# Optimization experiments

Measured on AMD Instinct MI355X. Metric: run time of the kernel, lower is better.

## Reference

```python
import jax, jax.numpy as jnp
import numpy as np

N = 100000      # nodes
E = 1600000     # edges (avg degree 16)
F_IN = 300      # input feature dim
H = 64          # hidden channels
OUT = 20        # output classes
L = 8           # num GCN2Conv layers
ALPHA = 0.1
THETA = 0.5


def setup_inputs() -> dict:
    key = jax.random.key(0)
    ks = jax.random.split(key, 6)
    x = jax.random.normal(ks[0], (N, F_IN), jnp.float32)
    edge_index = jax.random.randint(ks[1], (2, E), 0, N, dtype=jnp.int32)
    edge_weights = jax.random.uniform(ks[2], (E,), jnp.float32)
    W_in = jax.random.normal(ks[3], (F_IN, H), jnp.float32) / np.sqrt(F_IN)
    b_in = jnp.zeros((H,), jnp.float32)
    conv_w = jax.random.normal(ks[4], (L, H, H), jnp.float32) / np.sqrt(H)
    W_out = jax.random.normal(ks[5], (H, OUT), jnp.float32) / np.sqrt(H)
    b_out = jnp.zeros((OUT,), jnp.float32)
    return dict(x=x, edge_index=edge_index, edge_weights=edge_weights,
                W_in=W_in, b_in=b_in, conv_w=conv_w, W_out=W_out, b_out=b_out)


def _gcn_norm(edge_index, edge_weights, n, dtype):
    # add self-loops with weight 1, symmetric normalization (PyG gcn_norm)
    loop = jnp.arange(n, dtype=edge_index.dtype)
    row = jnp.concatenate([edge_index[0], loop])
    col = jnp.concatenate([edge_index[1], loop])
    w = jnp.concatenate([edge_weights, jnp.ones((n,), dtype)])
    deg = jax.ops.segment_sum(w, col, num_segments=n)
    dinv = jnp.where(deg > 0, jax.lax.rsqrt(deg), 0.0).astype(dtype)
    norm = dinv[row] * w * dinv[col]
    return row, col, norm


def reference(x, edge_index, edge_weights, W_in, b_in, conv_w, W_out, b_out):
    n = x.shape[0]
    row, col, norm = _gcn_norm(edge_index, edge_weights, n, x.dtype)
    # eval mode: dropout is identity
    h = jax.nn.relu(x @ W_in + b_in)   # start_with_lin (F_IN != H)
    x0 = h
    num_layers = conv_w.shape[0]
    for l in range(num_layers):
        beta = float(np.log(THETA / (l + 1) + 1.0))
        # A_hat @ h : gather sources, weight by norm, scatter-add to targets
        agg = jax.ops.segment_sum(norm[:, None] * h[row], col, num_segments=n)
        z = (1.0 - ALPHA) * agg + ALPHA * x0  # initial-residual mixing
        h = jax.nn.relu((1.0 - beta) * z + beta * (z @ conv_w[l]))
    return h @ W_out + b_out
```

## Files before the change

### kernel.cpp

```cpp
#include <hip/hip_runtime.h>
#include <hip/hip_fp16.h>
#include <math.h>


#define HID 64
#define FIN 300
#define NOUT 20
#define ALPHA 0.1f
#define DSCALE 262144.0f
#define CNT_SHIFT 25
#define DEG_MASK 0x1FFFFFFu

typedef _Float16 f16;
typedef f16 f16x8 __attribute__((ext_vector_type(8)));
typedef float f32x4 __attribute__((ext_vector_type(4)));

__device__ __forceinline__ float wdec(unsigned v) {
    union { unsigned short u; __half h; } c;
    c.u = (unsigned short)(v >> 17);
    return __half2float(c.h);
}

__global__ void accum_k(const int* __restrict__ row, const int* __restrict__ col,
                        const float* __restrict__ ew,
                        unsigned* __restrict__ packed,
                        uint2* __restrict__ rec, int e) {
    int i = blockIdx.x * blockDim.x + threadIdx.x;
    if (i < e) {
        int c = col[i], r = row[i];
        float wv = ew[i];
        unsigned q = (unsigned)__float2uint_rn(wv * DSCALE);
        unsigned old = atomicAdd(&packed[c], (1u << CNT_SHIFT) | q);
        unsigned rank = (old >> CNT_SHIFT) & 0x7Fu;
        union { __half h; unsigned short u; } cv;
        cv.h = __float2half(wv);
        rec[i] = make_uint2((unsigned)c | (rank << 17),
                            (unsigned)r | ((unsigned)cv.u << 17));
    }
}

__global__ __launch_bounds__(1024) void unpackscan_k(const unsigned* __restrict__ packed,
                                                     float* __restrict__ dinv,
                                                     int* __restrict__ padcnt,
                                                     int* __restrict__ bsum, int n) {
    __shared__ int ws[16];
    int t = threadIdx.x, i = blockIdx.x * 1024 + t;
    int pad = 0;
    if (i < n) {
        unsigned v = packed[i];
        int cnt = (int)(v >> CNT_SHIFT);
        float d = 1.0f + (float)(v & DEG_MASK) * (1.0f / DSCALE);
        dinv[i] = rsqrtf(d);
        pad = (cnt + 3) & ~3;
        padcnt[i] = pad;
    }
    int s = pad;
#pragma unroll
    for (int d = 1; d < 64; d <<= 1) s += __shfl_xor(s, d);
    if ((t & 63) == 0) ws[t >> 6] = s;
    __syncthreads();
    if (t == 0) {
        int tot = 0;
#pragma unroll
        for (int k = 0; k < 16; ++k) tot += ws[k];
        bsum[blockIdx.x] = tot;
    }
}

__global__ void scan2_k(int* __restrict__ bsum, int nb, int* __restrict__ rp, int n) {
    int lane = threadIdx.x;
    int acc = 0;
    for (int base = 0; base < nb; base += 64) {
        int idx = base + lane;
        int orig = (idx < nb) ? bsum[idx] : 0;
        int v = orig;
#pragma unroll
        for (int d = 1; d < 64; d <<= 1) {
            int u = __shfl_up(v, d);
            if (lane >= d) v += u;
        }
        if (idx < nb) bsum[idx] = acc + v - orig;
        acc += __shfl(v, 63);
    }
    if (lane == 0) rp[n] = acc;
}

__global__ __launch_bounds__(1024) void scan3_k(const int* __restrict__ padcnt,
                                                const int* __restrict__ bsum,
                                                int* __restrict__ rp, int n) {
    __shared__ int ws[16];
    int t = threadIdx.x, i = blockIdx.x * 1024 + t;
    int lane = t & 63, w = t >> 6;
    int v = (i < n) ? padcnt[i] : 0;
    int sv = v;
#pragma unroll
    for (int d = 1; d < 64; d <<= 1) {
        int u = __shfl_up(sv, d);
        if (lane >= d) sv += u;
    }
    if (lane == 63) ws[w] = sv;
    __syncthreads();
    if (w == 0) {
        int x = (lane < 16) ? ws[lane] : 0;
#pragma unroll
        for (int d = 1; d < 16; d <<= 1) {
            int u = __shfl_up(x, d);
            if (lane >= d) x += u;
        }
        if (lane < 16) ws[lane] = x;
    }
    __syncthreads();
    int woff = (w > 0) ? ws[w - 1] : 0;
    if (i < n) rp[i] = bsum[blockIdx.x] + woff + sv - v;
}

__global__ __launch_bounds__(256) void fill_k(const uint2* __restrict__ rec,
                                              const float* __restrict__ dinv,
                                              const int* __restrict__ rp,
                                              unsigned* __restrict__ edges,
                                              int e, int n) {
    int xcd = blockIdx.x & 7;
    int lo = (int)(((long long)n * xcd) >> 3);
    int hi = (int)(((long long)n * (xcd + 1)) >> 3);
    int nblk = gridDim.x >> 3;
    int stride = nblk * 256;
    for (int i = (blockIdx.x >> 3) * 256 + threadIdx.x; i < e; i += stride) {
        uint2 rc = rec[i];
        int c = (int)(rc.x & 0x1FFFFu);
        if (c < lo || c >= hi) continue;
        int r = (int)(rc.y & 0x1FFFFu);
        union { unsigned short u; __half h; } ev;
        ev.u = (unsigned short)(rc.y >> 17);
        float nw = (1.0f - ALPHA) * dinv[r] * __half2float(ev.h) * dinv[c];
        union { __half h; unsigned short u; } cv;
        cv.h = __float2half(nw);
        int rank = (int)((rc.x >> 17) & 0x7Fu);
        int pos = rp[c] + rank;
        edges[pos] = ((unsigned)cv.u << 17) | (unsigned)r;
    }
}

__global__ void wt_k(const float* __restrict__ Win, f16* __restrict__ Wt) {
    int i = blockIdx.x * blockDim.x + threadIdx.x;
    if (i < 64 * 320) {
        int c = i / 320, k = i - c * 320;
        Wt[i] = (k < FIN) ? (f16)Win[k * 64 + c] : (f16)0.0f;
    }
}

__global__ __launch_bounds__(256) void gemm_in_k(const float* __restrict__ x,
                                                 const f16* __restrict__ Wt,
                                                 const float* __restrict__ bin,
                                                 __half* __restrict__ x0h, int n) {
    __shared__ f16 As[64 * 72];
    int t = threadIdx.x, lane = t & 63, wv = t >> 6;
    int node0 = blockIdx.x * 64;
    int lr = lane & 15, kg = lane >> 4;
    int fi = t & 15, rowbase = t >> 4;
    f32x4 acc0 = {0, 0, 0, 0}, acc1 = {0, 0, 0, 0}, acc2 = {0, 0, 0, 0}, acc3 = {0, 0, 0, 0};
    float4 xr[4];

    auto loadchunk = [&](int c) {
#pragma unroll
        for (int it = 0; it < 4; ++it) {
            int row = rowbase + it * 16;
            int rr = node0 + row;
            rr = (rr < n) ? rr : (n - 1);
            int kbase = c * 64 + fi * 4;
            xr[it] = make_float4(0.f, 0.f, 0.f, 0.f);
            if (kbase < FIN)
                xr[it] = *reinterpret_cast<const float4*>(x + (size_t)rr * FIN + kbase);
        }
    };
    loadchunk(0);

    for (int c = 0; c < 5; ++c) {
        __syncthreads();
#pragma unroll
        for (int it = 0; it < 4; ++it) {
            int row = rowbase + it * 16;
            union { float2 f2; f16 h[4]; } u;
            u.h[0] = (f16)xr[it].x; u.h[1] = (f16)xr[it].y;
            u.h[2] = (f16)xr[it].z; u.h[3] = (f16)xr[it].w;
            *reinterpret_cast<float2*>(As + row * 72 + fi * 4) = u.f2;
        }
        __syncthreads();
        if (c < 4) loadchunk(c + 1);
#pragma unroll
        for (int ks = 0; ks < 2; ++ks) {
            f16x8 a = *(const f16x8*)(As + (wv * 16 + lr) * 72 + ks * 32 + kg * 8);
            const f16* wb = Wt + c * 64 + ks * 32 + kg * 8;
            f16x8 b0 = *(const f16x8*)(wb + (0 * 16 + lr) * 320);
            f16x8 b1 = *(const f16x8*)(wb + (1 * 16 + lr) * 320);
            f16x8 b2 = *(const f16x8*)(wb + (2 * 16 + lr) * 320);
            f16x8 b3 = *(const f16x8*)(wb + (3 * 16 + lr) * 320);
            acc0 = __builtin_amdgcn_mfma_f32_16x16x32_f16(a, b0, acc0, 0, 0, 0);
            acc1 = __builtin_amdgcn_mfma_f32_16x16x32_f16(a, b1, acc1, 0, 0, 0);
            acc2 = __builtin_amdgcn_mfma_f32_16x16x32_f16(a, b2, acc2, 0, 0, 0);
            acc3 = __builtin_amdgcn_mfma_f32_16x16x32_f16(a, b3, acc3, 0, 0, 0);
        }
    }
    float bi0 = bin[0 * 16 + lr], bi1 = bin[1 * 16 + lr];
    float bi2 = bin[2 * 16 + lr], bi3 = bin[3 * 16 + lr];
    f16 ov[4][4];
#pragma unroll
    for (int r = 0; r < 4; ++r) {
        ov[0][r] = (f16)fmaxf(acc0[r] + bi0, 0.f);
        ov[1][r] = (f16)fmaxf(acc1[r] + bi1, 0.f);
        ov[2][r] = (f16)fmaxf(acc2[r] + bi2, 0.f);
        ov[3][r] = (f16)fmaxf(acc3[r] + bi3, 0.f);
    }
    __syncthreads();
#pragma unroll
    for (int cg = 0; cg < 4; ++cg)
#pragma unroll
        for (int r = 0; r < 4; ++r)
            As[(wv * 16 + kg * 4 + r) * 72 + cg * 16 + lr] = ov[cg][r];
    __syncthreads();
#pragma unroll
    for (int it = 0; it < 2; ++it) {
        int idx = t + it * 256;
        int ch = idx & 3, nodel = (idx >> 2) & 63, q = idx >> 8;
        int node = node0 + nodel;
        if (node < n)
            *(float4*)((f16*)x0h + ((size_t)q * n + node) * 32 + ch * 8) =
                *reinterpret_cast<const float4*>(As + nodel * 72 + q * 32 + ch * 8);
    }
}

__global__ __launch_bounds__(256) void layer_k(const int* __restrict__ rp,
                                               const unsigned* __restrict__ edges,
                                               const float* __restrict__ dinv,
                                               const __half* __restrict__ x0h,
                                               const __half* __restrict__ hin,
                                               __half* __restrict__ hout,
                                               const float* __restrict__ Wl,
                                               float beta, int n,
                                               const float* __restrict__ Wout,
                                               const float* __restrict__ bout,
                                               float* __restrict__ out) {
    __shared__ f16 As[64 * 72];
    __shared__ f16 Bs[64 * 72];
    int t = threadIdx.x, lane = t & 63, wv = t >> 6;
    int node0 = blockIdx.x * 64;
    for (int i = t; i < 4096; i += 256) {
        int k = i >> 6, c = i & 63;
        Bs[c * 72 + k] = (f16)Wl[i];
    }
    int g = lane >> 2, s = lane & 3;
    int row = wv * 16 + g;
    int node = node0 + row;
    int nd = (node < n) ? node : (n - 1);
    int jbeg = rp[nd], end = (node < n) ? rp[nd + 1] : jbeg;
    float di = dinv[nd];
    float c1 = (1.0f - ALPHA) * di * di;
#pragma unroll
    for (int q = 0; q < 2; ++q) {
        const f16* hp = (const f16*)hin + (size_t)q * n * 32;
        const f16* xp = (const f16*)x0h + (size_t)q * n * 32;
        float a0[8], a1[8], a2[8], a3[8];
#pragma unroll
        for (int i = 0; i < 8; ++i) { a0[i] = 0.f; a1[i] = 0.f; a2[i] = 0.f; a3[i] = 0.f; }
        int j = jbeg;
        while (__any(j < end)) {
            if (j < end) {
                uint4 e4 = *reinterpret_cast<const uint4*>(edges + j);
                float w0 = wdec(e4.x), w1 = wdec(e4.y), w2 = wdec(e4.z), w3 = wdec(e4.w);
                f16x8 r0 = *(const f16x8*)(hp + (size_t)(e4.x & 0x1FFFF) * 32 + s * 8);
                f16x8 r1 = *(const f16x8*)(hp + (size_t)(e4.y & 0x1FFFF) * 32 + s * 8);
                f16x8 r2 = *(const f16x8*)(hp + (size_t)(e4.z & 0x1FFFF) * 32 + s * 8);
                f16x8 r3 = *(const f16x8*)(hp + (size_t)(e4.w & 0x1FFFF) * 32 + s * 8);
#pragma unroll
                for (int i = 0; i < 8; ++i) {
                    a0[i] = fmaf(w0, (float)r0[i], a0[i]);
                    a1[i] = fmaf(w1, (float)r1[i], a1[i]);
                    a2[i] = fmaf(w2, (float)r2[i], a2[i]);
                    a3[i] = fmaf(w3, (float)r3[i], a3[i]);
                }
            }
            j += 4;
        }
        f16x8 h8 = *(const f16x8*)(hp + (size_t)nd * 32 + s * 8);
        f16x8 x8 = *(const f16x8*)(xp + (size_t)nd * 32 + s * 8);
        f16x8 z8;
#pragma unroll
        for (int i = 0; i < 8; ++i)
            z8[i] = (f16)fmaf(ALPHA, (float)x8[i],
                              fmaf(c1, (float)h8[i], (a0[i] + a1[i]) + (a2[i] + a3[i])));
        *(f16x8*)(As + row * 72 + q * 32 + s * 8) = z8;
    }
    __syncthreads();
    int lr = lane & 15, kg = lane >> 4;
    f32x4 acc0 = {0, 0, 0, 0}, acc1 = {0, 0, 0, 0}, acc2 = {0, 0, 0, 0}, acc3 = {0, 0, 0, 0};
    f16x8 af0 = *(const f16x8*)(As + (wv * 16 + lr) * 72 + kg * 8);
    f16x8 af1 = *(const f16x8*)(As + (wv * 16 + lr) * 72 + 32 + kg * 8);
    {
        f16x8 b0 = *(const f16x8*)(Bs + (0 * 16 + lr) * 72 + kg * 8);
        f16x8 b1 = *(const f16x8*)(Bs + (0 * 16 + lr) * 72 + 32 + kg * 8);
        acc0 = __builtin_amdgcn_mfma_f32_16x16x32_f16(af0, b0, acc0, 0, 0, 0);
        acc0 = __builtin_amdgcn_mfma_f32_16x16x32_f16(af1, b1, acc0, 0, 0, 0);
    }
    {
        f16x8 b0 = *(const f16x8*)(Bs + (1 * 16 + lr) * 72 + kg * 8);
        f16x8 b1 = *(const f16x8*)(Bs + (1 * 16 + lr) * 72 + 32 + kg * 8);
        acc1 = __builtin_amdgcn_mfma_f32_16x16x32_f16(af0, b0, acc1, 0, 0, 0);
        acc1 = __builtin_amdgcn_mfma_f32_16x16x32_f16(af1, b1, acc1, 0, 0, 0);
    }
    {
        f16x8 b0 = *(const f16x8*)(Bs + (2 * 16 + lr) * 72 + kg * 8);
        f16x8 b1 = *(const f16x8*)(Bs + (2 * 16 + lr) * 72 + 32 + kg * 8);
        acc2 = __builtin_amdgcn_mfma_f32_16x16x32_f16(af0, b0, acc2, 0, 0, 0);
        acc2 = __builtin_amdgcn_mfma_f32_16x16x32_f16(af1, b1, acc2, 0, 0, 0);
    }
    {
        f16x8 b0 = *(const f16x8*)(Bs + (3 * 16 + lr) * 72 + kg * 8);
        f16x8 b1 = *(const f16x8*)(Bs + (3 * 16 + lr) * 72 + 32 + kg * 8);
        acc3 = __builtin_amdgcn_mfma_f32_16x16x32_f16(af0, b0, acc3, 0, 0, 0);
        acc3 = __builtin_amdgcn_mfma_f32_16x16x32_f16(af1, b1, acc3, 0, 0, 0);
    }
    float omb = 1.0f - beta;
    f16 ov[4][4];
#pragma unroll
    for (int cg = 0; cg < 4; ++cg) {
        f32x4 acc = (cg == 0) ? acc0 : (cg == 1) ? acc1 : (cg == 2) ? acc2 : acc3;
        int col = cg * 16 + lr;
#pragma unroll
        for (int r = 0; r < 4; ++r) {
            float zv = (float)As[(wv * 16 + kg * 4 + r) * 72 + col];
            ov[cg][r] = (f16)fmaxf(fmaf(beta, acc[r], omb * zv), 0.f);
        }
    }
    __syncthreads();
#pragma unroll
    for (int cg = 0; cg < 4; ++cg)
#pragma unroll
        for (int r = 0; r < 4; ++r)
            As[(wv * 16 + kg * 4 + r) * 72 + cg * 16 + lr] = ov[cg][r];
    __syncthreads();

    if (!Wout) {
#pragma unroll
        for (int it = 0; it < 2; ++it) {
            int idx = t + it * 256;
            int ch = idx & 3, nodel = (idx >> 2) & 63, q = idx >> 8;
            int nd2 = node0 + nodel;
            if (nd2 < n)
                *(float4*)((f16*)hout + ((size_t)q * n + nd2) * 32 + ch * 8) =
                    *reinterpret_cast<const float4*>(As + nodel * 72 + q * 32 + ch * 8);
        }
    } else {
        for (int i = t; i < 32 * 64; i += 256) {
            int c = i >> 6, k = i & 63;
            Bs[c * 72 + k] = (c < NOUT) ? (f16)Wout[k * NOUT + c] : (f16)0.0f;
        }
        __syncthreads();
        f16x8 ha0 = *(const f16x8*)(As + (wv * 16 + lr) * 72 + kg * 8);
        f16x8 ha1 = *(const f16x8*)(As + (wv * 16 + lr) * 72 + 32 + kg * 8);
#pragma unroll
        for (int ct = 0; ct < 2; ++ct) {
            f32x4 oacc = {0, 0, 0, 0};
            f16x8 b0 = *(const f16x8*)(Bs + (ct * 16 + lr) * 72 + kg * 8);
            f16x8 b1 = *(const f16x8*)(Bs + (ct * 16 + lr) * 72 + 32 + kg * 8);
            oacc = __builtin_amdgcn_mfma_f32_16x16x32_f16(ha0, b0, oacc, 0, 0, 0);
            oacc = __builtin_amdgcn_mfma_f32_16x16x32_f16(ha1, b1, oacc, 0, 0, 0);
            int col = ct * 16 + lr;
            if (col < NOUT) {
                float bo = bout[col];
#pragma unroll
                for (int r = 0; r < 4; ++r) {
                    int nd2 = node0 + wv * 16 + kg * 4 + r;
                    if (nd2 < n) out[(size_t)nd2 * NOUT + col] = oacc[r] + bo;
                }
            }
        }
    }
}

extern "C" void kernel_launch(void* const* d_in, const int* in_sizes, int n_in,
                              void* d_out, int out_size, void* d_ws, size_t ws_size,
                              hipStream_t stream) {
    const float* x    = (const float*)d_in[0];
    const int*   ei   = (const int*)d_in[1];
    const float* ew   = (const float*)d_in[2];
    const float* Win  = (const float*)d_in[3];
    const float* bin  = (const float*)d_in[4];
    const float* cw   = (const float*)d_in[5];
    const float* Wout = (const float*)d_in[6];
    const float* bout = (const float*)d_in[7];

    const int n = in_sizes[0] / FIN;
    const int e = in_sizes[2];
    const int L = in_sizes[5] / (HID * HID);
    const int* row = ei;
    const int* col = ei + e;
    const int epadmax = e + 3 * n + 64;

    size_t off = 0;
    auto alloc = [&](size_t bytes) -> char* {
        char* q = (char*)d_ws + off;
        off = (off + bytes + 255) & ~(size_t)255;
        return q;
    };
    __half* x0h  = (__half*)alloc((size_t)n * HID * 2);
    __half* hA   = (__half*)alloc((size_t)n * HID * 2);
    __half* hB   = (__half*)alloc((size_t)n * HID * 2);
    unsigned* edges = (unsigned*)alloc((size_t)epadmax * 4);
    uint2* rec   = (uint2*)alloc((size_t)e * 8);
    unsigned* packed = (unsigned*)alloc((size_t)n * 4);
    float* dinv  = (float*)alloc((size_t)n * 4);
    int*   padcnt= (int*)alloc((size_t)n * 4);
    int*   rp    = (int*)alloc((size_t)(n + 1) * 4);
    int*   bsum  = (int*)alloc(1024 * 4);
    f16*   Wt    = (f16*)alloc((size_t)64 * 320 * 2);

    const int nb = (n + 1023) / 1024;
    const int ntile = (n + 63) / 64;

    hipMemsetAsync(packed, 0, (size_t)n * 4, stream);
    hipMemsetAsync(edges, 0, (size_t)epadmax * 4, stream);
    accum_k<<<(e + 255) / 256, 256, 0, stream>>>(row, col, ew, packed, rec, e);
    unpackscan_k<<<nb, 1024, 0, stream>>>(packed, dinv, padcnt, bsum, n);
    scan2_k<<<1, 64, 0, stream>>>(bsum, nb, rp, n);
    scan3_k<<<nb, 1024, 0, stream>>>(padcnt, bsum, rp, n);
    fill_k<<<1024, 256, 0, stream>>>(rec, dinv, rp, edges, e, n);

    wt_k<<<(64 * 320 + 255) / 256, 256, 0, stream>>>(Win, Wt);
    gemm_in_k<<<ntile, 256, 0, stream>>>(x, Wt, bin, x0h, n);

    const __half* hin = x0h;
    __half* hout = hA;
    for (int l = 0; l < L; ++l) {
        float beta = (float)log(0.5 / (double)(l + 1) + 1.0);
        bool last = (l == L - 1);
        layer_k<<<ntile, 256, 0, stream>>>(rp, edges, dinv, x0h, hin, hout,
                                           cw + (size_t)l * HID * HID, beta, n,
                                           last ? Wout : nullptr,
                                           last ? bout : nullptr,
                                           last ? (float*)d_out : nullptr);
        hin = hout;
        hout = (hout == hA) ? hB : hA;
    }
}
```

Baseline: 568.9 us.

## Use row-major node features, XCD-partition accum, and fuse CSR fill with input GEMM

After: 490.0 us. 13.9% less time.

```diff
diff --git a/kernel.cpp b/kernel.cpp
--- a/kernel.cpp
+++ b/kernel.cpp
@@ -10,6 +10,7 @@
 #define DSCALE 262144.0f
 #define CNT_SHIFT 25
 #define DEG_MASK 0x1FFFFFFu
+#define FBLK 1024
 
 typedef _Float16 f16;
 typedef f16 f16x8 __attribute__((ext_vector_type(8)));
@@ -21,13 +22,30 @@
     return __half2float(c.h);
 }
 
-__global__ void accum_k(const int* __restrict__ row, const int* __restrict__ col,
-                        const float* __restrict__ ew,
-                        unsigned* __restrict__ packed,
-                        uint2* __restrict__ rec, int e) {
-    int i = blockIdx.x * blockDim.x + threadIdx.x;
-    if (i < e) {
-        int c = col[i], r = row[i];
+__device__ __forceinline__ void unpack8(const float4& v, float* f) {
+    const __half2* p = reinterpret_cast<const __half2*>(&v);
+#pragma unroll
+    for (int i = 0; i < 4; ++i) {
+        float2 t = __half22float2(p[i]);
+        f[2 * i] = t.x;
+        f[2 * i + 1] = t.y;
+    }
+}
+
+__global__ __launch_bounds__(256) void accum_k(const int* __restrict__ row,
+                                               const int* __restrict__ col,
+                                               const float* __restrict__ ew,
+                                               unsigned* __restrict__ packed,
+                                               uint2* __restrict__ rec, int e, int n) {
+    int xcd = blockIdx.x & 7;
+    int lo = (int)(((long long)n * xcd) >> 3);
+    int hi = (int)(((long long)n * (xcd + 1)) >> 3);
+    int nblk = gridDim.x >> 3;
+    int stride = nblk * 256;
+    for (int i = (blockIdx.x >> 3) * 256 + threadIdx.x; i < e; i += stride) {
+        int c = col[i];
+        if (c < lo || c >= hi) continue;
+        int r = row[i];
         float wv = ew[i];
         unsigned q = (unsigned)__float2uint_rn(wv * DSCALE);
         unsigned old = atomicAdd(&packed[c], (1u << CNT_SHIFT) | q);
@@ -114,32 +132,6 @@
     if (i < n) rp[i] = bsum[blockIdx.x] + woff + sv - v;
 }
 
-__global__ __launch_bounds__(256) void fill_k(const uint2* __restrict__ rec,
-                                              const float* __restrict__ dinv,
-                                              const int* __restrict__ rp,
-                                              unsigned* __restrict__ edges,
-                                              int e, int n) {
-    int xcd = blockIdx.x & 7;
-    int lo = (int)(((long long)n * xcd) >> 3);
-    int hi = (int)(((long long)n * (xcd + 1)) >> 3);
-    int nblk = gridDim.x >> 3;
-    int stride = nblk * 256;
-    for (int i = (blockIdx.x >> 3) * 256 + threadIdx.x; i < e; i += stride) {
-        uint2 rc = rec[i];
-        int c = (int)(rc.x & 0x1FFFFu);
-        if (c < lo || c >= hi) continue;
-        int r = (int)(rc.y & 0x1FFFFu);
-        union { unsigned short u; __half h; } ev;
-        ev.u = (unsigned short)(rc.y >> 17);
-        float nw = (1.0f - ALPHA) * dinv[r] * __half2float(ev.h) * dinv[c];
-        union { __half h; unsigned short u; } cv;
-        cv.h = __float2half(nw);
-        int rank = (int)((rc.x >> 17) & 0x7Fu);
-        int pos = rp[c] + rank;
-        edges[pos] = ((unsigned)cv.u << 17) | (unsigned)r;
-    }
-}
-
 __global__ void wt_k(const float* __restrict__ Win, f16* __restrict__ Wt) {
     int i = blockIdx.x * blockDim.x + threadIdx.x;
     if (i < 64 * 320) {
@@ -148,18 +140,42 @@
     }
 }
 
-__global__ __launch_bounds__(256) void gemm_in_k(const float* __restrict__ x,
-                                                 const f16* __restrict__ Wt,
-                                                 const float* __restrict__ bin,
-                                                 __half* __restrict__ x0h, int n) {
+__global__ __launch_bounds__(256) void fgi_k(const uint2* __restrict__ rec,
+                                             const float* __restrict__ dinv,
+                                             const int* __restrict__ rp,
+                                             unsigned* __restrict__ edges, int e,
+                                             const float* __restrict__ x,
+                                             const f16* __restrict__ Wt,
+                                             const float* __restrict__ bin,
+                                             __half* __restrict__ x0h, int n) {
     __shared__ f16 As[64 * 72];
-    int t = threadIdx.x, lane = t & 63, wv = t >> 6;
-    int node0 = blockIdx.x * 64;
+    int t = threadIdx.x;
+    if (blockIdx.x < FBLK) {
+        int xcd = blockIdx.x & 7;
+        int lo = (int)(((long long)n * xcd) >> 3);
+        int hi = (int)(((long long)n * (xcd + 1)) >> 3);
+        int stride = (FBLK >> 3) * 256;
+        for (int i = (blockIdx.x >> 3) * 256 + t; i < e; i += stride) {
+            uint2 rc = rec[i];
+            int c = (int)(rc.x & 0x1FFFFu);
+            if (c < lo || c >= hi) continue;
+            int r = (int)(rc.y & 0x1FFFFu);
+            union { unsigned short u; __half h; } ev;
+            ev.u = (unsigned short)(rc.y >> 17);
+            float nw = (1.0f - ALPHA) * dinv[r] * __half2float(ev.h) * dinv[c];
+            union { __half h; unsigned short u; } cv;
+            cv.h = __float2half(nw);
+            int rank = (int)((rc.x >> 17) & 0x7Fu);
+            edges[rp[c] + rank] = ((unsigned)cv.u << 17) | (unsigned)r;
+        }
+        return;
+    }
+    int lane = t & 63, wv = t >> 6;
+    int node0 = (blockIdx.x - FBLK) * 64;
     int lr = lane & 15, kg = lane >> 4;
     int fi = t & 15, rowbase = t >> 4;
     f32x4 acc0 = {0, 0, 0, 0}, acc1 = {0, 0, 0, 0}, acc2 = {0, 0, 0, 0}, acc3 = {0, 0, 0, 0};
     float4 xr[4];
-
     auto loadchunk = [&](int c) {
 #pragma unroll
         for (int it = 0; it < 4; ++it) {
@@ -173,7 +189,6 @@
         }
     };
     loadchunk(0);
-
     for (int c = 0; c < 5; ++c) {
         __syncthreads();
 #pragma unroll
@@ -220,11 +235,11 @@
 #pragma unroll
     for (int it = 0; it < 2; ++it) {
         int idx = t + it * 256;
-        int ch = idx & 3, nodel = (idx >> 2) & 63, q = idx >> 8;
-        int node = node0 + nodel;
+        int row = idx >> 3, ch = idx & 7;
+        int node = node0 + row;
         if (node < n)
-            *(float4*)((f16*)x0h + ((size_t)q * n + node) * 32 + ch * 8) =
-                *reinterpret_cast<const float4*>(As + nodel * 72 + q * 32 + ch * 8);
+            ((float4*)(x0h + (size_t)node * 64))[ch] =
+                *reinterpret_cast<const float4*>(As + row * 72 + ch * 8);
     }
 }
 
@@ -247,47 +262,52 @@
         int k = i >> 6, c = i & 63;
         Bs[c * 72 + k] = (f16)Wl[i];
     }
-    int g = lane >> 2, s = lane & 3;
-    int row = wv * 16 + g;
-    int node = node0 + row;
-    int nd = (node < n) ? node : (n - 1);
-    int jbeg = rp[nd], end = (node < n) ? rp[nd + 1] : jbeg;
-    float di = dinv[nd];
-    float c1 = (1.0f - ALPHA) * di * di;
-#pragma unroll
-    for (int q = 0; q < 2; ++q) {
-        const f16* hp = (const f16*)hin + (size_t)q * n * 32;
-        const f16* xp = (const f16*)x0h + (size_t)q * n * 32;
+    int g = lane >> 3, c8 = lane & 7;
+#pragma unroll
+    for (int pass = 0; pass < 2; ++pass) {
+        int row = pass * 32 + wv * 8 + g;
+        int node = node0 + row;
+        int nd = (node < n) ? node : (n - 1);
+        int j = rp[nd], end = (node < n) ? rp[nd + 1] : j;
         float a0[8], a1[8], a2[8], a3[8];
 #pragma unroll
         for (int i = 0; i < 8; ++i) { a0[i] = 0.f; a1[i] = 0.f; a2[i] = 0.f; a3[i] = 0.f; }
-        int j = jbeg;
         while (__any(j < end)) {
             if (j < end) {
                 uint4 e4 = *reinterpret_cast<const uint4*>(edges + j);
                 float w0 = wdec(e4.x), w1 = wdec(e4.y), w2 = wdec(e4.z), w3 = wdec(e4.w);
-                f16x8 r0 = *(const f16x8*)(hp + (size_t)(e4.x & 0x1FFFF) * 32 + s * 8);
-                f16x8 r1 = *(const f16x8*)(hp + (size_t)(e4.y & 0x1FFFF) * 32 + s * 8);
-                f16x8 r2 = *(const f16x8*)(hp + (size_t)(e4.z & 0x1FFFF) * 32 + s * 8);
-                f16x8 r3 = *(const f16x8*)(hp + (size_t)(e4.w & 0x1FFFF) * 32 + s * 8);
+                float4 r0 = ((const float4*)(hin + (size_t)(e4.x & 0x1FFFF) * 64))[c8];
+                float4 r1 = ((const float4*)(hin + (size_t)(e4.y & 0x1FFFF) * 64))[c8];
+                float4 r2 = ((const float4*)(hin + (size_t)(e4.z & 0x1FFFF) * 64))[c8];
+                float4 r3 = ((const float4*)(hin + (size_t)(e4.w & 0x1FFFF) * 64))[c8];
+                float f0[8], f1[8], f2[8], f3[8];
+                unpack8(r0, f0);
+                unpack8(r1, f1);
+                unpack8(r2, f2);
+                unpack8(r3, f3);
 #pragma unroll
                 for (int i = 0; i < 8; ++i) {
-                    a0[i] = fmaf(w0, (float)r0[i], a0[i]);
-                    a1[i] = fmaf(w1, (float)r1[i], a1[i]);
-                    a2[i] = fmaf(w2, (float)r2[i], a2[i]);
-                    a3[i] = fmaf(w3, (float)r3[i], a3[i]);
+                    a0[i] = fmaf(w0, f0[i], a0[i]);
+                    a1[i] = fmaf(w1, f1[i], a1[i]);
+                    a2[i] = fmaf(w2, f2[i], a2[i]);
+                    a3[i] = fmaf(w3, f3[i], a3[i]);
                 }
             }
             j += 4;
         }
-        f16x8 h8 = *(const f16x8*)(hp + (size_t)nd * 32 + s * 8);
-        f16x8 x8 = *(const f16x8*)(xp + (size_t)nd * 32 + s * 8);
-        f16x8 z8;
+        float di = dinv[nd];
+        float c1 = (1.0f - ALPHA) * di * di;
+        float4 hs4 = ((const float4*)(hin + (size_t)nd * 64))[c8];
+        float4 xs4 = ((const float4*)(x0h + (size_t)nd * 64))[c8];
+        float hf[8], xf[8];
+        unpack8(hs4, hf);
+        unpack8(xs4, xf);
+        f16x8 zv8;
 #pragma unroll
         for (int i = 0; i < 8; ++i)
-            z8[i] = (f16)fmaf(ALPHA, (float)x8[i],
-                              fmaf(c1, (float)h8[i], (a0[i] + a1[i]) + (a2[i] + a3[i])));
-        *(f16x8*)(As + row * 72 + q * 32 + s * 8) = z8;
+            zv8[i] = (f16)fmaf(ALPHA, xf[i],
+                               fmaf(c1, hf[i], (a0[i] + a1[i]) + (a2[i] + a3[i])));
+        *(f16x8*)(As + row * 72 + c8 * 8) = zv8;
     }
     __syncthreads();
     int lr = lane & 15, kg = lane >> 4;
@@ -342,11 +362,11 @@
 #pragma unroll
         for (int it = 0; it < 2; ++it) {
             int idx = t + it * 256;
-            int ch = idx & 3, nodel = (idx >> 2) & 63, q = idx >> 8;
-            int nd2 = node0 + nodel;
-            if (nd2 < n)
-                *(float4*)((f16*)hout + ((size_t)q * n + nd2) * 32 + ch * 8) =
-                    *reinterpret_cast<const float4*>(As + nodel * 72 + q * 32 + ch * 8);
+            int row = idx >> 3, ch = idx & 7;
+            int node = node0 + row;
+            if (node < n)
+                ((float4*)(hout + (size_t)node * 64))[ch] =
+                    *reinterpret_cast<const float4*>(As + row * 72 + ch * 8);
         }
     } else {
         for (int i = t; i < 32 * 64; i += 256) {
@@ -418,14 +438,14 @@
 
     hipMemsetAsync(packed, 0, (size_t)n * 4, stream);
     hipMemsetAsync(edges, 0, (size_t)epadmax * 4, stream);
-    accum_k<<<(e + 255) / 256, 256, 0, stream>>>(row, col, ew, packed, rec, e);
+    wt_k<<<(64 * 320 + 255) / 256, 256, 0, stream>>>(Win, Wt);
+    accum_k<<<1024, 256, 0, stream>>>(row, col, ew, packed, rec, e, n);
     unpackscan_k<<<nb, 1024, 0, stream>>>(packed, dinv, padcnt, bsum, n);
     scan2_k<<<1, 64, 0, stream>>>(bsum, nb, rp, n);
     scan3_k<<<nb, 1024, 0, stream>>>(padcnt, bsum, rp, n);
-    fill_k<<<1024, 256, 0, stream>>>(rec, dinv, rp, edges, e, n);
-
-    wt_k<<<(64 * 320 + 255) / 256, 256, 0, stream>>>(Win, Wt);
-    gemm_in_k<<<ntile, 256, 0, stream>>>(x, Wt, bin, x0h, n);
+
+    fgi_k<<<FBLK + ntile, 256, 0, stream>>>(rec, dinv, rp, edges, e,
+                                            x, Wt, bin, x0h, n);
 
     const __half* hin = x0h;
     __half* hout = hA;
```
